# Optimization experiments

Measured on AMD Instinct MI355X. Metric: run time of the kernel, lower is better.

The kernel has to match this reference:

```python
import jax, jax.numpy as jnp
import numpy as np


def setup_inputs() -> dict:
    key0 = jax.random.key(0)
    kq, kk, kv = jax.random.split(key0, 3)
    B, S, D = 16, 2048, 64  # batch*heads, seq_len, head_dim
    return {
        "query": jax.random.normal(kq, (B, S, D), dtype=jnp.float32),
        "key": jax.random.normal(kk, (B, S, D), dtype=jnp.float32),
        "value": jax.random.normal(kv, (B, S, D), dtype=jnp.float32),
    }


def reference(query, key, value):
    # context = K @ V^T : [B, S, S]  (the seq x seq intermediate the kernel should avoid)
    context = jnp.einsum("bkd,bvd->bkv", key, value)
    # attention = context^T @ Q : [B, S, D]
    attention = jnp.einsum("bkv,bkd->bvd", context, query)
    return attention
```

## Files before the change

kernel.cpp:

```cpp
#include <hip/hip_runtime.h>


typedef float vf4 __attribute__((ext_vector_type(4)));

#define BATCH 16
#define SEQ   2048
#define DIM   64
#define SCHUNK 128
#define NCHUNK (SEQ / SCHUNK)
#define ROWS2  128

__global__ __launch_bounds__(256) void ktq_part_kernel(
        const float* __restrict__ K, const float* __restrict__ Q,
        float* __restrict__ P) {
    const int b     = blockIdx.y;
    const int chunk = blockIdx.x;
    const int t     = threadIdx.x;
    const int tx    = t & 15;
    const int ty    = t >> 4;

    const float* Kb = K + ((size_t)b * SEQ + (size_t)chunk * SCHUNK) * DIM + ty * 4;
    const float* Qb = Q + ((size_t)b * SEQ + (size_t)chunk * SCHUNK) * DIM + tx * 4;

    float acc[4][4] = {};
#pragma unroll 8
    for (int s = 0; s < SCHUNK; ++s) {
        vf4 ak = *(const vf4*)&Kb[s * DIM];
        vf4 bq = *(const vf4*)&Qb[s * DIM];
#pragma unroll
        for (int i = 0; i < 4; ++i)
#pragma unroll
            for (int j = 0; j < 4; ++j) acc[i][j] += ak[i] * bq[j];
    }

    float* Pb = P + ((size_t)b * NCHUNK + chunk) * DIM * DIM;
#pragma unroll
    for (int i = 0; i < 4; ++i) {
        vf4 r = {acc[i][0], acc[i][1], acc[i][2], acc[i][3]};
        *(vf4*)&Pb[(ty * 4 + i) * DIM + tx * 4] = r;
    }
}

__global__ __launch_bounds__(512) void vm_red_kernel(
        const float* __restrict__ V, const float* __restrict__ P,
        float* __restrict__ O) {
    __shared__ __attribute__((aligned(16))) float Ml[DIM * DIM];
    const int b  = blockIdx.y;
    const int rb = blockIdx.x;
    const int t  = threadIdx.x;

    const float* Pb = P + (size_t)b * NCHUNK * DIM * DIM;
#pragma unroll
    for (int i = 0; i < 2; ++i) {
        int idx = i * 512 + t;
        vf4 sum = ((const vf4*)Pb)[idx];
#pragma unroll
        for (int c = 1; c < NCHUNK; ++c)
            sum += ((const vf4*)(Pb + (size_t)c * DIM * DIM))[idx];
        ((vf4*)Ml)[idx] = sum;
    }
    __syncthreads();

    const int tx = t & 15;
    const int ty = t >> 4;
    const float* Vb = V + ((size_t)b * SEQ + (size_t)rb * ROWS2 + ty * 4) * DIM;

    float acc[4][4] = {};
#pragma unroll 4
    for (int dpc = 0; dpc < DIM / 4; ++dpc) {
        vf4 m0 = *(const vf4*)&Ml[(dpc * 4 + 0) * DIM + tx * 4];
        vf4 m1 = *(const vf4*)&Ml[(dpc * 4 + 1) * DIM + tx * 4];
        vf4 m2 = *(const vf4*)&Ml[(dpc * 4 + 2) * DIM + tx * 4];
        vf4 m3 = *(const vf4*)&Ml[(dpc * 4 + 3) * DIM + tx * 4];
#pragma unroll
        for (int i = 0; i < 4; ++i) {
            vf4 v = *(const vf4*)&Vb[i * DIM + dpc * 4];
#pragma unroll
            for (int j = 0; j < 4; ++j) {
                acc[i][j] += v[0] * m0[j] + v[1] * m1[j]
                           + v[2] * m2[j] + v[3] * m3[j];
            }
        }
    }

    float* Ob = O + ((size_t)b * SEQ + (size_t)rb * ROWS2) * DIM;
#pragma unroll
    for (int i = 0; i < 4; ++i) {
        vf4 o = {acc[i][0], acc[i][1], acc[i][2], acc[i][3]};
        __builtin_nontemporal_store(o, (vf4*)&Ob[(ty * 4 + i) * DIM + tx * 4]);
    }
}

extern "C" void kernel_launch(void* const* d_in, const int* in_sizes, int n_in,
                              void* d_out, int out_size, void* d_ws, size_t ws_size,
                              hipStream_t stream) {
    const float* Q = (const float*)d_in[0];
    const float* K = (const float*)d_in[1];
    const float* V = (const float*)d_in[2];
    float* O = (float*)d_out;
    float* P = (float*)d_ws;

    dim3 gridA(NCHUNK, BATCH);
    ktq_part_kernel<<<gridA, 256, 0, stream>>>(K, Q, P);

    dim3 gridB(SEQ / ROWS2, BATCH);
    vm_red_kernel<<<gridB, 512, 0, stream>>>(V, P, O);
}
```

Before: 96.54 us.

## Stage K/Q and transposed V in LDS with larger register tiles and split-K reduction

The first kernel now copies each chunk of K and Q into shared memory and gives each wave a quarter of the sequence rows. Each thread computes an 8x8 outer-product tile, and the four waves' partial results are summed through shared memory. The second kernel transposes the V tile into padded shared memory and splits the 64-wide inner dimension across two thread halves with a 4x8 register tile, adding the halves before the store. This raises arithmetic per load and removes strided global reads, at the cost of more LDS traffic, extra barriers, more registers and possibly lower occupancy.

Result: faster. 88.65 us (-8.2%).

```diff
diff --git a/kernel.cpp b/kernel.cpp
--- a/kernel.cpp
+++ b/kernel.cpp
@@ -8,46 +8,88 @@
 #define DIM   64
 #define SCHUNK 128
 #define NCHUNK (SEQ / SCHUNK)
+#define SW     (SCHUNK / 4)
 #define ROWS2  128
+#define TPADR  132
+#define RSTRA  68
+#define RSTRB  36
 
 __global__ __launch_bounds__(256) void ktq_part_kernel(
         const float* __restrict__ K, const float* __restrict__ Q,
         float* __restrict__ P) {
-    const int b     = blockIdx.y;
-    const int chunk = blockIdx.x;
-    const int t     = threadIdx.x;
-    const int tx    = t & 15;
-    const int ty    = t >> 4;
+    __shared__ __attribute__((aligned(16))) float Sm[2 * SCHUNK * DIM];
+    float* Ks = Sm;
+    float* Qs = Sm + SCHUNK * DIM;
+    const int b = blockIdx.y, chunk = blockIdx.x, t = threadIdx.x;
+    const int w = t >> 6, l = t & 63;
 
-    const float* Kb = K + ((size_t)b * SEQ + (size_t)chunk * SCHUNK) * DIM + ty * 4;
-    const float* Qb = Q + ((size_t)b * SEQ + (size_t)chunk * SCHUNK) * DIM + tx * 4;
-
-    float acc[4][4] = {};
-#pragma unroll 8
-    for (int s = 0; s < SCHUNK; ++s) {
-        vf4 ak = *(const vf4*)&Kb[s * DIM];
-        vf4 bq = *(const vf4*)&Qb[s * DIM];
+    const size_t rowbase = ((size_t)b * SEQ + (size_t)chunk * SCHUNK + (size_t)w * SW) * DIM;
+    const vf4* Kg = (const vf4*)(K + rowbase);
+    const vf4* Qg = (const vf4*)(Q + rowbase);
+    vf4* KsW = (vf4*)(Ks + w * SW * DIM);
+    vf4* QsW = (vf4*)(Qs + w * SW * DIM);
 #pragma unroll
-        for (int i = 0; i < 4; ++i)
-#pragma unroll
-            for (int j = 0; j < 4; ++j) acc[i][j] += ak[i] * bq[j];
+    for (int j = 0; j < 8; ++j) {
+        KsW[j * 64 + l] = Kg[j * 64 + l];
+        QsW[j * 64 + l] = Qg[j * 64 + l];
     }
 
-    float* Pb = P + ((size_t)b * NCHUNK + chunk) * DIM * DIM;
+    const int tx = l & 7, ty = l >> 3;
+    const float* KsR = Ks + w * SW * DIM + ty * 8;
+    const float* QsR = Qs + w * SW * DIM + tx * 8;
+    float acc[8][8] = {};
+#pragma unroll 2
+    for (int s = 0; s < SW; ++s) {
+        vf4 a0 = *(const vf4*)&KsR[s * DIM];
+        vf4 a1 = *(const vf4*)&KsR[s * DIM + 4];
+        vf4 b0 = *(const vf4*)&QsR[s * DIM];
+        vf4 b1 = *(const vf4*)&QsR[s * DIM + 4];
+        float a[8]  = {a0[0], a0[1], a0[2], a0[3], a1[0], a1[1], a1[2], a1[3]};
+        float bb[8] = {b0[0], b0[1], b0[2], b0[3], b1[0], b1[1], b1[2], b1[3]};
 #pragma unroll
-    for (int i = 0; i < 4; ++i) {
-        vf4 r = {acc[i][0], acc[i][1], acc[i][2], acc[i][3]};
-        *(vf4*)&Pb[(ty * 4 + i) * DIM + tx * 4] = r;
+        for (int i = 0; i < 8; ++i)
+#pragma unroll
+            for (int j = 0; j < 8; ++j) acc[i][j] += a[i] * bb[j];
+    }
+
+    __syncthreads();
+    if (w != 0) {
+        float* Rs = Sm + (size_t)(w - 1) * 64 * RSTRA + l * RSTRA;
+#pragma unroll
+        for (int i = 0; i < 8; ++i) {
+            vf4 r0 = {acc[i][0], acc[i][1], acc[i][2], acc[i][3]};
+            vf4 r1 = {acc[i][4], acc[i][5], acc[i][6], acc[i][7]};
+            *(vf4*)&Rs[i * 8]     = r0;
+            *(vf4*)&Rs[i * 8 + 4] = r1;
+        }
+    }
+    __syncthreads();
+    if (w == 0) {
+        float* Pb = P + ((size_t)b * NCHUNK + chunk) * DIM * DIM
+                  + (size_t)(ty * 8) * DIM + tx * 8;
+#pragma unroll
+        for (int i = 0; i < 8; ++i) {
+#pragma unroll
+            for (int jh = 0; jh < 2; ++jh) {
+                vf4 sum = {acc[i][jh * 4 + 0], acc[i][jh * 4 + 1],
+                           acc[i][jh * 4 + 2], acc[i][jh * 4 + 3]};
+#pragma unroll
+                for (int p = 0; p < 3; ++p)
+                    sum += *(const vf4*)&Sm[(size_t)p * 64 * RSTRA + l * RSTRA
+                                            + i * 8 + jh * 4];
+                *(vf4*)&Pb[i * DIM + jh * 4] = sum;
+            }
+        }
     }
 }
 
 __global__ __launch_bounds__(512) void vm_red_kernel(
         const float* __restrict__ V, const float* __restrict__ P,
         float* __restrict__ O) {
-    __shared__ __attribute__((aligned(16))) float Ml[DIM * DIM];
-    const int b  = blockIdx.y;
-    const int rb = blockIdx.x;
-    const int t  = threadIdx.x;
+    __shared__ __attribute__((aligned(16))) float Sm[DIM * DIM + DIM * TPADR];
+    float* Ml  = Sm;
+    float* VsT = Sm + DIM * DIM;
+    const int b = blockIdx.y, rb = blockIdx.x, t = threadIdx.x;
 
     const float* Pb = P + (size_t)b * NCHUNK * DIM * DIM;
 #pragma unroll
@@ -59,35 +101,66 @@
             sum += ((const vf4*)(Pb + (size_t)c * DIM * DIM))[idx];
         ((vf4*)Ml)[idx] = sum;
     }
+
+    const float* Vb = V + ((size_t)b * SEQ + (size_t)rb * ROWS2) * DIM;
+    {
+        const int r0 = (t >> 4) * 4;
+        const int c0 = (t & 15) * 4;
+        vf4 tmp[4];
+#pragma unroll
+        for (int r = 0; r < 4; ++r)
+            tmp[r] = *(const vf4*)&Vb[(size_t)(r0 + r) * DIM + c0];
+#pragma unroll
+        for (int c = 0; c < 4; ++c) {
+            vf4 wv = {tmp[0][c], tmp[1][c], tmp[2][c], tmp[3][c]};
+            *(vf4*)&VsT[(size_t)(c0 + c) * TPADR + r0] = wv;
+        }
+    }
     __syncthreads();
 
-    const int tx = t & 15;
-    const int ty = t >> 4;
-    const float* Vb = V + ((size_t)b * SEQ + (size_t)rb * ROWS2 + ty * 4) * DIM;
+    const int g = t >> 8, sub = t & 255;
+    const int tx = sub & 7, ty = sub >> 3;
+    float acc[4][8] = {};
+#pragma unroll 2
+    for (int d0 = 0; d0 < 32; ++d0) {
+        const int dp = g * 32 + d0;
+        vf4 m0 = *(const vf4*)&Ml[dp * DIM + tx * 8];
+        vf4 m1 = *(const vf4*)&Ml[dp * DIM + tx * 8 + 4];
+        vf4 av = *(const vf4*)&VsT[dp * TPADR + ty * 4];
+        float m[8] = {m0[0], m0[1], m0[2], m0[3], m1[0], m1[1], m1[2], m1[3]};
+#pragma unroll
+        for (int i = 0; i < 4; ++i)
+#pragma unroll
+            for (int j = 0; j < 8; ++j) acc[i][j] += av[i] * m[j];
+    }
 
-    float acc[4][4] = {};
-#pragma unroll 4
-    for (int dpc = 0; dpc < DIM / 4; ++dpc) {
-        vf4 m0 = *(const vf4*)&Ml[(dpc * 4 + 0) * DIM + tx * 4];
-        vf4 m1 = *(const vf4*)&Ml[(dpc * 4 + 1) * DIM + tx * 4];
-        vf4 m2 = *(const vf4*)&Ml[(dpc * 4 + 2) * DIM + tx * 4];
-        vf4 m3 = *(const vf4*)&Ml[(dpc * 4 + 3) * DIM + tx * 4];
+    __syncthreads();
+    if (g == 1) {
+        float* Rs = Sm + (size_t)sub * RSTRB;
 #pragma unroll
         for (int i = 0; i < 4; ++i) {
-            vf4 v = *(const vf4*)&Vb[i * DIM + dpc * 4];
+            vf4 r0 = {acc[i][0], acc[i][1], acc[i][2], acc[i][3]};
+            vf4 r1 = {acc[i][4], acc[i][5], acc[i][6], acc[i][7]};
+            *(vf4*)&Rs[i * 8]     = r0;
+            *(vf4*)&Rs[i * 8 + 4] = r1;
+        }
+    }
+    __syncthreads();
+    if (g == 0) {
+        const float* Rs = Sm + (size_t)sub * RSTRB;
+        float* Ob = O + ((size_t)b * SEQ + (size_t)rb * ROWS2 + (size_t)ty * 4) * DIM
+                  + tx * 8;
 #pragma unroll
-            for (int j = 0; j < 4; ++j) {
-                acc[i][j] += v[0] * m0[j] + v[1] * m1[j]
-                           + v[2] * m2[j] + v[3] * m3[j];
+        for (int i = 0; i < 4; ++i) {
+#pragma unroll
+            for (int jh = 0; jh < 2; ++jh) {
+                vf4 s0 = {acc[i][jh * 4 + 0], acc[i][jh * 4 + 1],
+                          acc[i][jh * 4 + 2], acc[i][jh * 4 + 3]};
+                vf4 s1 = *(const vf4*)&Rs[i * 8 + jh * 4];
+                vf4 o = s0 + s1;
+                __builtin_nontemporal_store(o, (vf4*)&Ob[i * DIM + jh * 4]);
             }
         }
-    }
-
-    float* Ob = O + ((size_t)b * SEQ + (size_t)rb * ROWS2) * DIM;
-#pragma unroll
-    for (int i = 0; i < 4; ++i) {
-        vf4 o = {acc[i][0], acc[i][1], acc[i][2], acc[i][3]};
-        __builtin_nontemporal_store(o, (vf4*)&Ob[(ty * 4 + i) * DIM + tx * 4]);
     }
 }
 
```
